# Kernel tuning notes

Hardware: AMD Instinct MI355X
Metric: run time of the kernel (lower is better)

Reference implementation:

```python
import jax, jax.numpy as jnp
import numpy as np

N_NODES = 100000
N_EDGES = 1600000
IN_CH = 64 * 2  # 128


def setup_inputs() -> dict:
    key = jax.random.key(0)
    ks = jax.random.split(key, 10)
    x = jax.random.normal(ks[0], (N_NODES, IN_CH), dtype=jnp.float32)
    edge_index = jax.random.randint(ks[1], (2, N_EDGES), 0, N_NODES, dtype=jnp.int64)
    # PyTorch Linear default init scale ~ 1/sqrt(fan_in); plain normals are fine for a numeric reference
    W1 = jax.random.normal(ks[2], (IN_CH, 64), dtype=jnp.float32) / np.sqrt(IN_CH)
    b1 = jax.random.normal(ks[3], (64,), dtype=jnp.float32) * 0.01
    W2 = jax.random.normal(ks[4], (64, 64), dtype=jnp.float32) / np.sqrt(64)
    b2 = jax.random.normal(ks[5], (64,), dtype=jnp.float32) * 0.01
    W3 = jax.random.normal(ks[6], (64, 16), dtype=jnp.float32) / np.sqrt(64)
    b3 = jax.random.normal(ks[7], (16,), dtype=jnp.float32) * 0.01
    W4 = jax.random.normal(ks[8], (16, 1), dtype=jnp.float32) / np.sqrt(16)
    b4 = jax.random.normal(ks[9], (1,), dtype=jnp.float32) * 0.01
    return {"x": x, "edge_index": edge_index, "W1": W1, "b1": b1, "W2": W2, "b2": b2,
            "W3": W3, "b3": b3, "W4": W4, "b4": b4}


def _gin_agg(h, src, dst, n):
    # GINConv (eps=0, add aggregation): x_i + sum_{j->i} x_j
    return h + jax.ops.segment_sum(h[src], dst, num_segments=n)


def reference(x, edge_index, W1, b1, W2, b2, W3, b3, W4, b4):
    src, dst = edge_index[0], edge_index[1]
    n = x.shape[0]
    h = jax.nn.relu(_gin_agg(x, src, dst, n) @ W1 + b1)   # conv1 + relu -> [N, 64]
    h = jax.nn.relu(_gin_agg(h, src, dst, n) @ W2 + b2)   # conv2 + relu -> [N, 64]
    h = jax.nn.relu(h @ W3 + b3)                          # lin1 + relu  -> [N, 16]
    return h @ W4 + b4                                    # lin2         -> [N, 1]
```

## Files before the change

### kernel.cpp

```cpp
#include <hip/hip_runtime.h>
#include <hip/hip_fp16.h>

#define N_NODES 100000
#define N_EDGES 1600000
#define NBUCK 196
#define BUCAP 10240
#define P1_EDGES 8192
#define NP1 196
#define CURPAD 32

typedef _Float16 f16x8 __attribute__((ext_vector_type(8)));
typedef float    f32x4 __attribute__((ext_vector_type(4)));

__global__ __launch_bounds__(256) void k_zero_cur(int* __restrict__ cursor) {
    if (threadIdx.x < NBUCK) cursor[threadIdx.x * CURPAD] = 0;
}

__global__ __launch_bounds__(1024) void k_p1(const int* __restrict__ ei,
                                             int* __restrict__ cursor,
                                             int* __restrict__ bArr) {
    __shared__ int hist[NBUCK];
    const int tid = threadIdx.x;
    if (tid < NBUCK) hist[tid] = 0;

    const int eb = blockIdx.x * P1_EDGES;
    int d[8], s[8];
    #pragma unroll
    for (int j = 0; j < 2; ++j) {
        const int e = eb + j * 4096 + tid * 4;
        if (e < N_EDGES) {
            int4 dd = *(const int4*)&ei[N_EDGES + e];
            int4 ss = *(const int4*)&ei[e];
            d[j*4+0] = dd.x; d[j*4+1] = dd.y; d[j*4+2] = dd.z; d[j*4+3] = dd.w;
            s[j*4+0] = ss.x; s[j*4+1] = ss.y; s[j*4+2] = ss.z; s[j*4+3] = ss.w;
        } else {
            d[j*4+0] = -1; d[j*4+1] = -1; d[j*4+2] = -1; d[j*4+3] = -1;
            s[j*4+0] = 0;  s[j*4+1] = 0;  s[j*4+2] = 0;  s[j*4+3] = 0;
        }
    }
    __syncthreads();
    #pragma unroll
    for (int j = 0; j < 8; ++j)
        if (d[j] >= 0) atomicAdd(&hist[d[j] >> 9], 1);
    __syncthreads();
    if (tid < NBUCK) {
        int c = hist[tid];
        int base = atomicAdd(&cursor[tid * CURPAD], c);
        hist[tid] = base;
    }
    __syncthreads();
    #pragma unroll
    for (int j = 0; j < 8; ++j)
        if (d[j] >= 0) {
            int bk  = d[j] >> 9;
            int pos = atomicAdd(&hist[bk], 1);
            if (pos < BUCAP)
                bArr[bk * BUCAP + pos] = ((d[j] & 511) << 17) | s[j];
        }
}

__global__ __launch_bounds__(1024) void k_p2(const int* __restrict__ bArr,
                                             const int* __restrict__ cursor,
                                             int* __restrict__ srcS,
                                             int* __restrict__ off) {
    __shared__ int hist[512];
    __shared__ int wtot[8];
    __shared__ int curL[NBUCK];
    __shared__ int ordered[BUCAP];
    const int tid = threadIdx.x;
    const int b   = blockIdx.x;
    if (tid < 512)   hist[tid] = 0;
    if (tid < NBUCK) curL[tid] = cursor[tid * CURPAD];
    __syncthreads();

    int n = curL[b]; if (n > BUCAP) n = BUCAP;
    int gBase = 0;
    for (int j = 0; j < NBUCK; ++j) gBase += (j < b) ? curL[j] : 0;

    int pk[10];
    #pragma unroll
    for (int j = 0; j < 10; ++j) {
        int i = tid + j * 1024;
        pk[j] = (i < n) ? bArr[b * BUCAP + i] : -1;
    }
    #pragma unroll
    for (int j = 0; j < 10; ++j)
        if (pk[j] >= 0) atomicAdd(&hist[pk[j] >> 17], 1);
    __syncthreads();

    int v = 0, incl = 0;
    if (tid < 512) {
        v = hist[tid]; incl = v;
        #pragma unroll
        for (int dd = 1; dd < 64; dd <<= 1) {
            int t = __shfl_up(incl, dd, 64);
            if ((tid & 63) >= dd) incl += t;
        }
        if ((tid & 63) == 63) wtot[tid >> 6] = incl;
    }
    __syncthreads();
    if (tid < 512) {
        int add = 0;
        #pragma unroll
        for (int w = 0; w < 8; ++w) add += (w < (tid >> 6)) ? wtot[w] : 0;
        int ex = add + incl - v;
        hist[tid] = ex;
        int node = b * 512 + tid;
        if (node < N_NODES) off[node] = gBase + ex;
    }
    if (b == NBUCK - 1 && tid == 0) off[N_NODES] = N_EDGES;
    __syncthreads();

    #pragma unroll
    for (int j = 0; j < 10; ++j)
        if (pk[j] >= 0) {
            int dl  = pk[j] >> 17;
            int pos = atomicAdd(&hist[dl], 1);
            ordered[pos] = pk[j] & 0x1FFFF;
        }
    __syncthreads();
    for (int i = tid; i < n; i += 1024) srcS[gBase + i] = ordered[i];
}

__device__ __forceinline__ float2 gather_core(const int* __restrict__ off,
                                              const int* __restrict__ srcS,
                                              const __half* __restrict__ y16,
                                              int node, int lane) {
    const int hf   = lane >> 5;
    const int ln32 = lane & 31;
    const int beg = off[node];
    const int end = off[node + 1];

    float2 acc = {0.f, 0.f};
    if (hf == 0) {
        __half2 hv = *(const __half2*)&y16[((size_t)node << 6) + (ln32 << 1)];
        float2 f = __half22float2(hv);
        acc.x = f.x; acc.y = f.y;
    }

    int i = beg;
    while (i < end) {
        const int rem  = end - i;
        const int take = rem < 64 ? rem : 64;
        int idx = i + lane;
        if (idx > end - 1) idx = end - 1;
        const int sv = srcS[idx];
        int j = 0;
        for (; j + 16 <= take; j += 16) {
            const int s0 = __shfl(sv, j + 0  + hf), s1 = __shfl(sv, j + 2  + hf);
            const int s2 = __shfl(sv, j + 4  + hf), s3 = __shfl(sv, j + 6  + hf);
            const int s4 = __shfl(sv, j + 8  + hf), s5 = __shfl(sv, j + 10 + hf);
            const int s6 = __shfl(sv, j + 12 + hf), s7 = __shfl(sv, j + 14 + hf);
            const __half2 h0 = *(const __half2*)&y16[((size_t)s0 << 6) + (ln32 << 1)];
            const __half2 h1 = *(const __half2*)&y16[((size_t)s1 << 6) + (ln32 << 1)];
            const __half2 h2 = *(const __half2*)&y16[((size_t)s2 << 6) + (ln32 << 1)];
            const __half2 h3 = *(const __half2*)&y16[((size_t)s3 << 6) + (ln32 << 1)];
            const __half2 h4 = *(const __half2*)&y16[((size_t)s4 << 6) + (ln32 << 1)];
            const __half2 h5 = *(const __half2*)&y16[((size_t)s5 << 6) + (ln32 << 1)];
            const __half2 h6 = *(const __half2*)&y16[((size_t)s6 << 6) + (ln32 << 1)];
            const __half2 h7 = *(const __half2*)&y16[((size_t)s7 << 6) + (ln32 << 1)];
            float2 f0 = __half22float2(h0), f1 = __half22float2(h1);
            float2 f2 = __half22float2(h2), f3 = __half22float2(h3);
            float2 f4 = __half22float2(h4), f5 = __half22float2(h5);
            float2 f6 = __half22float2(h6), f7 = __half22float2(h7);
            acc.x += ((f0.x + f1.x) + (f2.x + f3.x)) + ((f4.x + f5.x) + (f6.x + f7.x));
            acc.y += ((f0.y + f1.y) + (f2.y + f3.y)) + ((f4.y + f5.y) + (f6.y + f7.y));
        }
        for (; j + 2 <= take; j += 2) {
            const int s = __shfl(sv, j + hf);
            const __half2 hv = *(const __half2*)&y16[((size_t)s << 6) + (ln32 << 1)];
            float2 f = __half22float2(hv);
            acc.x += f.x; acc.y += f.y;
        }
        if (j < take) {
            const int s = __shfl(sv, j);
            if (hf == 0) {
                const __half2 hv = *(const __half2*)&y16[((size_t)s << 6) + (ln32 << 1)];
                float2 f = __half22float2(hv);
                acc.x += f.x; acc.y += f.y;
            }
        }
        i += take;
    }
    return acc;
}

__global__ __launch_bounds__(256) void k_gather_h1(const int* __restrict__ off,
                                                   const int* __restrict__ srcS,
                                                   const __half* __restrict__ y16,
                                                   const float* __restrict__ b1,
                                                   __half* __restrict__ h16) {
    const int node = blockIdx.x * 4 + (threadIdx.x >> 6);
    if (node >= N_NODES) return;
    const int lane = threadIdx.x & 63;
    const int hf = lane >> 5, ln32 = lane & 31;
    float2 bb = {0.f, 0.f};
    if (hf == 0) bb = *(const float2*)&b1[ln32 * 2];

    float2 acc = gather_core(off, srcS, y16, node, lane);
    acc.x += __shfl_xor(acc.x, 32, 64);
    acc.y += __shfl_xor(acc.y, 32, 64);
    if (hf == 0) {
        float hx = fmaxf(acc.x + bb.x, 0.f);
        float hy = fmaxf(acc.y + bb.y, 0.f);
        *(__half2*)&h16[((size_t)node << 6) + (ln32 << 1)] = __floats2half2_rn(hx, hy);
    }
}

__global__ __launch_bounds__(256) void k_gather_tail(const int* __restrict__ off,
                                                     const int* __restrict__ srcS,
                                                     const __half* __restrict__ y16,
                                                     const float* __restrict__ b2,
                                                     const float* __restrict__ W3,
                                                     const float* __restrict__ b3,
                                                     const float* __restrict__ W4,
                                                     const float* __restrict__ b4,
                                                     float* __restrict__ out) {
    __shared__ float sh2[4][64];
    const int wv   = threadIdx.x >> 6;
    const int node = blockIdx.x * 4 + wv;
    if (node >= N_NODES) return;
    const int lane = threadIdx.x & 63;
    const int hf = lane >> 5, ln32 = lane & 31;

    const int jj = lane & 15, pp = lane >> 4;
    float w3r[16];
    #pragma unroll
    for (int k = 0; k < 16; ++k) w3r[k] = W3[(pp * 16 + k) * 16 + jj];
    const float b3j = b3[jj], w4j = W4[jj], b4v = b4[0];
    float2 bb = {0.f, 0.f};
    if (hf == 0) bb = *(const float2*)&b2[ln32 * 2];

    float2 acc = gather_core(off, srcS, y16, node, lane);
    acc.x += __shfl_xor(acc.x, 32, 64);
    acc.y += __shfl_xor(acc.y, 32, 64);
    if (hf == 0) {
        float hx = fmaxf(acc.x + bb.x, 0.f);
        float hy = fmaxf(acc.y + bb.y, 0.f);
        *(float2*)&sh2[wv][ln32 * 2] = make_float2(hx, hy);
    }
    const float4 hA = *(const float4*)&sh2[wv][pp * 16 + 0];
    const float4 hB = *(const float4*)&sh2[wv][pp * 16 + 4];
    const float4 hC = *(const float4*)&sh2[wv][pp * 16 + 8];
    const float4 hD = *(const float4*)&sh2[wv][pp * 16 + 12];
    float part = hA.x * w3r[0]  + hA.y * w3r[1]  + hA.z * w3r[2]  + hA.w * w3r[3]
               + hB.x * w3r[4]  + hB.y * w3r[5]  + hB.z * w3r[6]  + hB.w * w3r[7]
               + hC.x * w3r[8]  + hC.y * w3r[9]  + hC.z * w3r[10] + hC.w * w3r[11]
               + hD.x * w3r[12] + hD.y * w3r[13] + hD.z * w3r[14] + hD.w * w3r[15];
    part += __shfl_xor(part, 16, 64);
    part += __shfl_xor(part, 32, 64);
    float o = fmaxf(part + b3j, 0.f) * w4j;
    o += __shfl_xor(o, 1, 64);
    o += __shfl_xor(o, 2, 64);
    o += __shfl_xor(o, 4, 64);
    o += __shfl_xor(o, 8, 64);
    if (lane == 0) out[node] = o + b4v;
}

__global__ __launch_bounds__(256) void k_mm1(const float* __restrict__ x,
                                             const float* __restrict__ W1,
                                             __half* __restrict__ y16) {
    __shared__ __half sB[64 * 136];
    const int tid = threadIdx.x;
    for (int i = tid * 4; i < 128 * 64; i += 1024) {
        int k = i >> 6, n = i & 63;
        float4 w = *(const float4*)&W1[i];
        sB[(n + 0) * 136 + k] = __float2half(w.x);
        sB[(n + 1) * 136 + k] = __float2half(w.y);
        sB[(n + 2) * 136 + k] = __float2half(w.z);
        sB[(n + 3) * 136 + k] = __float2half(w.w);
    }
    __syncthreads();
    const int wv = tid >> 6, l = tid & 63;
    const int row0 = blockIdx.x * 64 + wv * 16;
    int arow = row0 + (l & 15);
    if (arow >= N_NODES) arow = N_NODES - 1;
    const int kgrp = (l >> 4) * 8;

    f32x4 acc0 = {0,0,0,0}, acc1 = {0,0,0,0}, acc2 = {0,0,0,0}, acc3 = {0,0,0,0};
    #pragma unroll
    for (int ks = 0; ks < 4; ++ks) {
        const float4 a0 = *(const float4*)&x[(size_t)arow * 128 + ks * 32 + kgrp];
        const float4 a1 = *(const float4*)&x[(size_t)arow * 128 + ks * 32 + kgrp + 4];
        f16x8 af;
        af[0] = (_Float16)a0.x; af[1] = (_Float16)a0.y;
        af[2] = (_Float16)a0.z; af[3] = (_Float16)a0.w;
        af[4] = (_Float16)a1.x; af[5] = (_Float16)a1.y;
        af[6] = (_Float16)a1.z; af[7] = (_Float16)a1.w;
        union { uint4 u; f16x8 h; } B0, B1, B2, B3;
        B0.u = *(const uint4*)&sB[(0 * 16 + (l & 15)) * 136 + ks * 32 + kgrp];
        B1.u = *(const uint4*)&sB[(1 * 16 + (l & 15)) * 136 + ks * 32 + kgrp];
        B2.u = *(const uint4*)&sB[(2 * 16 + (l & 15)) * 136 + ks * 32 + kgrp];
        B3.u = *(const uint4*)&sB[(3 * 16 + (l & 15)) * 136 + ks * 32 + kgrp];
        acc0 = __builtin_amdgcn_mfma_f32_16x16x32_f16(af, B0.h, acc0, 0, 0, 0);
        acc1 = __builtin_amdgcn_mfma_f32_16x16x32_f16(af, B1.h, acc1, 0, 0, 0);
        acc2 = __builtin_amdgcn_mfma_f32_16x16x32_f16(af, B2.h, acc2, 0, 0, 0);
        acc3 = __builtin_amdgcn_mfma_f32_16x16x32_f16(af, B3.h, acc3, 0, 0, 0);
    }
    #pragma unroll
    for (int rr = 0; rr < 4; ++rr) {
        const int orow = row0 + (l >> 4) * 4 + rr;
        if (orow < N_NODES) {
            __half* yp = &y16[(size_t)orow * 64 + (l & 15)];
            yp[0]  = __float2half(acc0[rr]);
            yp[16] = __float2half(acc1[rr]);
            yp[32] = __float2half(acc2[rr]);
            yp[48] = __float2half(acc3[rr]);
        }
    }
}

__global__ __launch_bounds__(256) void k_mm2(const __half* __restrict__ h16,
                                             const float* __restrict__ W2,
                                             __half* __restrict__ y16) {
    __shared__ __half sB[64 * 72];
    const int tid = threadIdx.x;
    for (int i = tid * 4; i < 64 * 64; i += 1024) {
        int k = i >> 6, n = i & 63;
        float4 w = *(const float4*)&W2[i];
        sB[(n + 0) * 72 + k] = __float2half(w.x);
        sB[(n + 1) * 72 + k] = __float2half(w.y);
        sB[(n + 2) * 72 + k] = __float2half(w.z);
        sB[(n + 3) * 72 + k] = __float2half(w.w);
    }
    __syncthreads();
    const int wv = tid >> 6, l = tid & 63;
    const int row0 = blockIdx.x * 64 + wv * 16;
    int arow = row0 + (l & 15);
    if (arow >= N_NODES) arow = N_NODES - 1;
    const int kgrp = (l >> 4) * 8;

    f32x4 acc0 = {0,0,0,0}, acc1 = {0,0,0,0}, acc2 = {0,0,0,0}, acc3 = {0,0,0,0};
    #pragma unroll
    for (int ks = 0; ks < 2; ++ks) {
        union { uint4 u; f16x8 h; } A;
        A.u = *(const uint4*)&h16[(size_t)arow * 64 + ks * 32 + kgrp];
        union { uint4 u; f16x8 h; } B0, B1, B2, B3;
        B0.u = *(const uint4*)&sB[(0 * 16 + (l & 15)) * 72 + ks * 32 + kgrp];
        B1.u = *(const uint4*)&sB[(1 * 16 + (l & 15)) * 72 + ks * 32 + kgrp];
        B2.u = *(const uint4*)&sB[(2 * 16 + (l & 15)) * 72 + ks * 32 + kgrp];
        B3.u = *(const uint4*)&sB[(3 * 16 + (l & 15)) * 72 + ks * 32 + kgrp];
        acc0 = __builtin_amdgcn_mfma_f32_16x16x32_f16(A.h, B0.h, acc0, 0, 0, 0);
        acc1 = __builtin_amdgcn_mfma_f32_16x16x32_f16(A.h, B1.h, acc1, 0, 0, 0);
        acc2 = __builtin_amdgcn_mfma_f32_16x16x32_f16(A.h, B2.h, acc2, 0, 0, 0);
        acc3 = __builtin_amdgcn_mfma_f32_16x16x32_f16(A.h, B3.h, acc3, 0, 0, 0);
    }
    #pragma unroll
    for (int rr = 0; rr < 4; ++rr) {
        const int orow = row0 + (l >> 4) * 4 + rr;
        if (orow < N_NODES) {
            __half* yp = &y16[(size_t)orow * 64 + (l & 15)];
            yp[0]  = __float2half(acc0[rr]);
            yp[16] = __float2half(acc1[rr]);
            yp[32] = __float2half(acc2[rr]);
            yp[48] = __float2half(acc3[rr]);
        }
    }
}

extern "C" void kernel_launch(void* const* d_in, const int* in_sizes, int n_in,
                              void* d_out, int out_size, void* d_ws, size_t ws_size,
                              hipStream_t stream) {
    const float* x  = (const float*)d_in[0];
    const int*   ei = (const int*)d_in[1];
    const float* W1 = (const float*)d_in[2];
    const float* b1 = (const float*)d_in[3];
    const float* W2 = (const float*)d_in[4];
    const float* b2 = (const float*)d_in[5];
    const float* W3 = (const float*)d_in[6];
    const float* b3 = (const float*)d_in[7];
    const float* W4 = (const float*)d_in[8];
    const float* b4 = (const float*)d_in[9];
    float* out = (float*)d_out;

    __half* h16    = (__half*)d_ws;
    __half* y16    = h16 + (size_t)N_NODES * 64;
    int*    off    = (int*)(y16 + (size_t)N_NODES * 64);
    int*    srcS   = off + N_NODES + 4;
    int*    cursor = srcS + N_EDGES;
    int*    bArr   = (int*)d_ws;

    const int mmBlocks  = (N_NODES + 63) / 64;
    const int aggBlocks = (N_NODES + 3) / 4;

    k_zero_cur<<<1, 256, 0, stream>>>(cursor);
    k_p1<<<NP1, 1024, 0, stream>>>(ei, cursor, bArr);
    k_p2<<<NBUCK, 1024, 0, stream>>>(bArr, cursor, srcS, off);

    k_mm1<<<mmBlocks, 256, 0, stream>>>(x, W1, y16);
    k_gather_h1<<<aggBlocks, 256, 0, stream>>>(off, srcS, y16, b1, h16);
    k_mm2<<<mmBlocks, 256, 0, stream>>>(h16, W2, y16);
    k_gather_tail<<<aggBlocks, 256, 0, stream>>>(off, srcS, y16, b2, W3, b3, W4, b4, out);
}
```

Before: 254.9 us.

## Stage bucketed edges in LDS for coalesced scatter, use fp16 pair adds in gather

```diff
diff --git a/kernel.cpp b/kernel.cpp
--- a/kernel.cpp
+++ b/kernel.cpp
@@ -5,8 +5,8 @@
 #define N_EDGES 1600000
 #define NBUCK 196
 #define BUCAP 10240
-#define P1_EDGES 8192
-#define NP1 196
+#define P1_EDGES 4096
+#define NP1 391
 #define CURPAD 32
 
 typedef _Float16 f16x8 __attribute__((ext_vector_type(8)));
@@ -20,43 +20,54 @@
                                              int* __restrict__ cursor,
                                              int* __restrict__ bArr) {
     __shared__ int hist[NBUCK];
+    __shared__ int lcur[NBUCK];
+    __shared__ int gdb[NBUCK];
+    __shared__ int lim[NBUCK];
+    __shared__ int stage[P1_EDGES];
+    __shared__ int sdest[P1_EDGES];
+    __shared__ int sTot;
     const int tid = threadIdx.x;
     if (tid < NBUCK) hist[tid] = 0;
 
-    const int eb = blockIdx.x * P1_EDGES;
-    int d[8], s[8];
-    #pragma unroll
-    for (int j = 0; j < 2; ++j) {
-        const int e = eb + j * 4096 + tid * 4;
-        if (e < N_EDGES) {
-            int4 dd = *(const int4*)&ei[N_EDGES + e];
-            int4 ss = *(const int4*)&ei[e];
-            d[j*4+0] = dd.x; d[j*4+1] = dd.y; d[j*4+2] = dd.z; d[j*4+3] = dd.w;
-            s[j*4+0] = ss.x; s[j*4+1] = ss.y; s[j*4+2] = ss.z; s[j*4+3] = ss.w;
-        } else {
-            d[j*4+0] = -1; d[j*4+1] = -1; d[j*4+2] = -1; d[j*4+3] = -1;
-            s[j*4+0] = 0;  s[j*4+1] = 0;  s[j*4+2] = 0;  s[j*4+3] = 0;
-        }
-    }
-    __syncthreads();
-    #pragma unroll
-    for (int j = 0; j < 8; ++j)
+    const int e = blockIdx.x * P1_EDGES + tid * 4;
+    int4 dd = {-1, -1, -1, -1}, ss = {0, 0, 0, 0};
+    if (e < N_EDGES) {
+        dd = *(const int4*)&ei[N_EDGES + e];
+        ss = *(const int4*)&ei[e];
+    }
+    __syncthreads();
+    int d[4] = {dd.x, dd.y, dd.z, dd.w};
+    int s[4] = {ss.x, ss.y, ss.z, ss.w};
+    #pragma unroll
+    for (int j = 0; j < 4; ++j)
         if (d[j] >= 0) atomicAdd(&hist[d[j] >> 9], 1);
     __syncthreads();
     if (tid < NBUCK) {
-        int c = hist[tid];
-        int base = atomicAdd(&cursor[tid * CURPAD], c);
-        hist[tid] = base;
-    }
-    __syncthreads();
-    #pragma unroll
-    for (int j = 0; j < 8; ++j)
+        int c  = hist[tid];
+        int lb = 0;
+        for (int j = 0; j < NBUCK; ++j) lb += (j < tid) ? hist[j] : 0;
+        if (tid == NBUCK - 1) sTot = lb + c;
+        int g = atomicAdd(&cursor[tid * CURPAD], c);
+        lcur[tid] = lb;
+        gdb[tid]  = tid * BUCAP + g - lb;
+        lim[tid]  = tid * BUCAP + BUCAP;
+    }
+    __syncthreads();
+    #pragma unroll
+    for (int j = 0; j < 4; ++j)
         if (d[j] >= 0) {
-            int bk  = d[j] >> 9;
-            int pos = atomicAdd(&hist[bk], 1);
-            if (pos < BUCAP)
-                bArr[bk * BUCAP + pos] = ((d[j] & 511) << 17) | s[j];
-        }
+            int bk   = d[j] >> 9;
+            int lpos = atomicAdd(&lcur[bk], 1);
+            int dest = gdb[bk] + lpos;
+            stage[lpos] = ((d[j] & 511) << 17) | s[j];
+            sdest[lpos] = (dest < lim[bk]) ? dest : -1;
+        }
+    __syncthreads();
+    const int tot = sTot;
+    for (int i = tid; i < tot; i += 1024) {
+        int dst = sdest[i];
+        if (dst >= 0) bArr[dst] = stage[i];
+    }
 }
 
 __global__ __launch_bounds__(1024) void k_p2(const int* __restrict__ bArr,
@@ -128,12 +139,14 @@
                                               int node, int lane) {
     const int hf   = lane >> 5;
     const int ln32 = lane & 31;
+    const unsigned co = (unsigned)(ln32 << 2);
+    const char* yb = (const char*)y16;
     const int beg = off[node];
     const int end = off[node + 1];
 
     float2 acc = {0.f, 0.f};
     if (hf == 0) {
-        __half2 hv = *(const __half2*)&y16[((size_t)node << 6) + (ln32 << 1)];
+        __half2 hv = *(const __half2*)(yb + (((unsigned)node << 7) | co));
         float2 f = __half22float2(hv);
         acc.x = f.x; acc.y = f.y;
     }
@@ -151,31 +164,33 @@
             const int s2 = __shfl(sv, j + 4  + hf), s3 = __shfl(sv, j + 6  + hf);
             const int s4 = __shfl(sv, j + 8  + hf), s5 = __shfl(sv, j + 10 + hf);
             const int s6 = __shfl(sv, j + 12 + hf), s7 = __shfl(sv, j + 14 + hf);
-            const __half2 h0 = *(const __half2*)&y16[((size_t)s0 << 6) + (ln32 << 1)];
-            const __half2 h1 = *(const __half2*)&y16[((size_t)s1 << 6) + (ln32 << 1)];
-            const __half2 h2 = *(const __half2*)&y16[((size_t)s2 << 6) + (ln32 << 1)];
-            const __half2 h3 = *(const __half2*)&y16[((size_t)s3 << 6) + (ln32 << 1)];
-            const __half2 h4 = *(const __half2*)&y16[((size_t)s4 << 6) + (ln32 << 1)];
-            const __half2 h5 = *(const __half2*)&y16[((size_t)s5 << 6) + (ln32 << 1)];
-            const __half2 h6 = *(const __half2*)&y16[((size_t)s6 << 6) + (ln32 << 1)];
-            const __half2 h7 = *(const __half2*)&y16[((size_t)s7 << 6) + (ln32 << 1)];
-            float2 f0 = __half22float2(h0), f1 = __half22float2(h1);
-            float2 f2 = __half22float2(h2), f3 = __half22float2(h3);
-            float2 f4 = __half22float2(h4), f5 = __half22float2(h5);
-            float2 f6 = __half22float2(h6), f7 = __half22float2(h7);
-            acc.x += ((f0.x + f1.x) + (f2.x + f3.x)) + ((f4.x + f5.x) + (f6.x + f7.x));
-            acc.y += ((f0.y + f1.y) + (f2.y + f3.y)) + ((f4.y + f5.y) + (f6.y + f7.y));
+            const __half2 h0 = *(const __half2*)(yb + (((unsigned)s0 << 7) | co));
+            const __half2 h1 = *(const __half2*)(yb + (((unsigned)s1 << 7) | co));
+            const __half2 h2 = *(const __half2*)(yb + (((unsigned)s2 << 7) | co));
+            const __half2 h3 = *(const __half2*)(yb + (((unsigned)s3 << 7) | co));
+            const __half2 h4 = *(const __half2*)(yb + (((unsigned)s4 << 7) | co));
+            const __half2 h5 = *(const __half2*)(yb + (((unsigned)s5 << 7) | co));
+            const __half2 h6 = *(const __half2*)(yb + (((unsigned)s6 << 7) | co));
+            const __half2 h7 = *(const __half2*)(yb + (((unsigned)s7 << 7) | co));
+            const __half2 t0 = __hadd2(h0, h1);
+            const __half2 t1 = __hadd2(h2, h3);
+            const __half2 t2 = __hadd2(h4, h5);
+            const __half2 t3 = __hadd2(h6, h7);
+            float2 f0 = __half22float2(t0), f1 = __half22float2(t1);
+            float2 f2 = __half22float2(t2), f3 = __half22float2(t3);
+            acc.x += (f0.x + f1.x) + (f2.x + f3.x);
+            acc.y += (f0.y + f1.y) + (f2.y + f3.y);
         }
         for (; j + 2 <= take; j += 2) {
             const int s = __shfl(sv, j + hf);
-            const __half2 hv = *(const __half2*)&y16[((size_t)s << 6) + (ln32 << 1)];
+            const __half2 hv = *(const __half2*)(yb + (((unsigned)s << 7) | co));
             float2 f = __half22float2(hv);
             acc.x += f.x; acc.y += f.y;
         }
         if (j < take) {
             const int s = __shfl(sv, j);
             if (hf == 0) {
-                const __half2 hv = *(const __half2*)&y16[((size_t)s << 6) + (ln32 << 1)];
+                const __half2 hv = *(const __half2*)(yb + (((unsigned)s << 7) | co));
                 float2 f = __half22float2(hv);
                 acc.x += f.x; acc.y += f.y;
             }
```

New measurement: 250.8 us. Within noise of the previous version (-1.6%).

## Co-schedule CSR bucket sort with first matmul in one launch

Applied to the files above, without the earlier changes.

```diff
diff --git a/kernel.cpp b/kernel.cpp
--- a/kernel.cpp
+++ b/kernel.cpp
@@ -7,14 +7,11 @@
 #define BUCAP 10240
 #define P1_EDGES 8192
 #define NP1 196
+#define MM1_BLOCKS 391
 #define CURPAD 32
 
 typedef _Float16 f16x8 __attribute__((ext_vector_type(8)));
 typedef float    f32x4 __attribute__((ext_vector_type(4)));
-
-__global__ __launch_bounds__(256) void k_zero_cur(int* __restrict__ cursor) {
-    if (threadIdx.x < NBUCK) cursor[threadIdx.x * CURPAD] = 0;
-}
 
 __global__ __launch_bounds__(1024) void k_p1(const int* __restrict__ ei,
                                              int* __restrict__ cursor,
@@ -59,67 +56,120 @@
         }
 }
 
-__global__ __launch_bounds__(1024) void k_p2(const int* __restrict__ bArr,
-                                             const int* __restrict__ cursor,
-                                             int* __restrict__ srcS,
-                                             int* __restrict__ off) {
-    __shared__ int hist[512];
-    __shared__ int wtot[8];
-    __shared__ int curL[NBUCK];
-    __shared__ int ordered[BUCAP];
+__global__ __launch_bounds__(1024) void k_p2mm1(const int* __restrict__ bArr,
+                                                const int* __restrict__ cursor,
+                                                int* __restrict__ srcS,
+                                                int* __restrict__ off,
+                                                const float* __restrict__ x,
+                                                const float* __restrict__ W1,
+                                                __half* __restrict__ y16) {
+    __shared__ union SU {
+        struct { int hist[512]; int wtot[8]; int curL[NBUCK]; int ordered[BUCAP]; } p2;
+        __half sB[64 * 136];
+    } u;
     const int tid = threadIdx.x;
-    const int b   = blockIdx.x;
-    if (tid < 512)   hist[tid] = 0;
-    if (tid < NBUCK) curL[tid] = cursor[tid * CURPAD];
-    __syncthreads();
-
-    int n = curL[b]; if (n > BUCAP) n = BUCAP;
-    int gBase = 0;
-    for (int j = 0; j < NBUCK; ++j) gBase += (j < b) ? curL[j] : 0;
-
-    int pk[10];
-    #pragma unroll
-    for (int j = 0; j < 10; ++j) {
-        int i = tid + j * 1024;
-        pk[j] = (i < n) ? bArr[b * BUCAP + i] : -1;
-    }
-    #pragma unroll
-    for (int j = 0; j < 10; ++j)
-        if (pk[j] >= 0) atomicAdd(&hist[pk[j] >> 17], 1);
-    __syncthreads();
-
-    int v = 0, incl = 0;
-    if (tid < 512) {
-        v = hist[tid]; incl = v;
-        #pragma unroll
-        for (int dd = 1; dd < 64; dd <<= 1) {
-            int t = __shfl_up(incl, dd, 64);
-            if ((tid & 63) >= dd) incl += t;
-        }
-        if ((tid & 63) == 63) wtot[tid >> 6] = incl;
-    }
-    __syncthreads();
-    if (tid < 512) {
-        int add = 0;
-        #pragma unroll
-        for (int w = 0; w < 8; ++w) add += (w < (tid >> 6)) ? wtot[w] : 0;
-        int ex = add + incl - v;
-        hist[tid] = ex;
-        int node = b * 512 + tid;
-        if (node < N_NODES) off[node] = gBase + ex;
-    }
-    if (b == NBUCK - 1 && tid == 0) off[N_NODES] = N_EDGES;
-    __syncthreads();
-
-    #pragma unroll
-    for (int j = 0; j < 10; ++j)
-        if (pk[j] >= 0) {
-            int dl  = pk[j] >> 17;
-            int pos = atomicAdd(&hist[dl], 1);
-            ordered[pos] = pk[j] & 0x1FFFF;
-        }
-    __syncthreads();
-    for (int i = tid; i < n; i += 1024) srcS[gBase + i] = ordered[i];
+
+    if (blockIdx.x < NBUCK) {
+        const int b = blockIdx.x;
+        if (tid < 512)   u.p2.hist[tid] = 0;
+        if (tid < NBUCK) u.p2.curL[tid] = cursor[tid * CURPAD];
+        __syncthreads();
+
+        int n = u.p2.curL[b]; if (n > BUCAP) n = BUCAP;
+        int gBase = 0;
+        for (int j = 0; j < NBUCK; ++j) gBase += (j < b) ? u.p2.curL[j] : 0;
+
+        int pk[10];
+        #pragma unroll
+        for (int j = 0; j < 10; ++j) {
+            int i = tid + j * 1024;
+            pk[j] = (i < n) ? bArr[b * BUCAP + i] : -1;
+        }
+        #pragma unroll
+        for (int j = 0; j < 10; ++j)
+            if (pk[j] >= 0) atomicAdd(&u.p2.hist[pk[j] >> 17], 1);
+        __syncthreads();
+
+        int v = 0, incl = 0;
+        if (tid < 512) {
+            v = u.p2.hist[tid]; incl = v;
+            #pragma unroll
+            for (int dd = 1; dd < 64; dd <<= 1) {
+                int t = __shfl_up(incl, dd, 64);
+                if ((tid & 63) >= dd) incl += t;
+            }
+            if ((tid & 63) == 63) u.p2.wtot[tid >> 6] = incl;
+        }
+        __syncthreads();
+        if (tid < 512) {
+            int add = 0;
+            #pragma unroll
+            for (int w = 0; w < 8; ++w) add += (w < (tid >> 6)) ? u.p2.wtot[w] : 0;
+            int ex = add + incl - v;
+            u.p2.hist[tid] = ex;
+            int node = b * 512 + tid;
+            if (node < N_NODES) off[node] = gBase + ex;
+        }
+        if (b == NBUCK - 1 && tid == 0) off[N_NODES] = N_EDGES;
+        __syncthreads();
+
+        #pragma unroll
+        for (int j = 0; j < 10; ++j)
+            if (pk[j] >= 0) {
+                int dl  = pk[j] >> 17;
+                int pos = atomicAdd(&u.p2.hist[dl], 1);
+                u.p2.ordered[pos] = pk[j] & 0x1FFFF;
+            }
+        __syncthreads();
+        for (int i = tid; i < n; i += 1024) srcS[gBase + i] = u.p2.ordered[i];
+    } else {
+        for (int i = tid * 4; i < 128 * 64; i += 4096) {
+            int k = i >> 6, nn = i & 63;
+            float4 w = *(const float4*)&W1[i];
+            u.sB[(nn + 0) * 136 + k] = __float2half(w.x);
+            u.sB[(nn + 1) * 136 + k] = __float2half(w.y);
+            u.sB[(nn + 2) * 136 + k] = __float2half(w.z);
+            u.sB[(nn + 3) * 136 + k] = __float2half(w.w);
+        }
+        __syncthreads();
+        const int wv = tid >> 6, l = tid & 63;
+        const int row0 = (blockIdx.x - NBUCK) * 256 + wv * 16;
+        int arow = row0 + (l & 15);
+        if (arow >= N_NODES) arow = N_NODES - 1;
+        const int kgrp = (l >> 4) * 8;
+
+        f32x4 acc0 = {0,0,0,0}, acc1 = {0,0,0,0}, acc2 = {0,0,0,0}, acc3 = {0,0,0,0};
+        #pragma unroll
+        for (int ks = 0; ks < 4; ++ks) {
+            const float4 a0 = *(const float4*)&x[(size_t)arow * 128 + ks * 32 + kgrp];
+            const float4 a1 = *(const float4*)&x[(size_t)arow * 128 + ks * 32 + kgrp + 4];
+            f16x8 af;
+            af[0] = (_Float16)a0.x; af[1] = (_Float16)a0.y;
+            af[2] = (_Float16)a0.z; af[3] = (_Float16)a0.w;
+            af[4] = (_Float16)a1.x; af[5] = (_Float16)a1.y;
+            af[6] = (_Float16)a1.z; af[7] = (_Float16)a1.w;
+            union { uint4 q; f16x8 h; } B0, B1, B2, B3;
+            B0.q = *(const uint4*)&u.sB[(0 * 16 + (l & 15)) * 136 + ks * 32 + kgrp];
+            B1.q = *(const uint4*)&u.sB[(1 * 16 + (l & 15)) * 136 + ks * 32 + kgrp];
+            B2.q = *(const uint4*)&u.sB[(2 * 16 + (l & 15)) * 136 + ks * 32 + kgrp];
+            B3.q = *(const uint4*)&u.sB[(3 * 16 + (l & 15)) * 136 + ks * 32 + kgrp];
+            acc0 = __builtin_amdgcn_mfma_f32_16x16x32_f16(af, B0.h, acc0, 0, 0, 0);
+            acc1 = __builtin_amdgcn_mfma_f32_16x16x32_f16(af, B1.h, acc1, 0, 0, 0);
+            acc2 = __builtin_amdgcn_mfma_f32_16x16x32_f16(af, B2.h, acc2, 0, 0, 0);
+            acc3 = __builtin_amdgcn_mfma_f32_16x16x32_f16(af, B3.h, acc3, 0, 0, 0);
+        }
+        #pragma unroll
+        for (int rr = 0; rr < 4; ++rr) {
+            const int orow = row0 + (l >> 4) * 4 + rr;
+            if (orow < N_NODES) {
+                __half* yp = &y16[(size_t)orow * 64 + (l & 15)];
+                yp[0]  = __float2half(acc0[rr]);
+                yp[16] = __float2half(acc1[rr]);
+                yp[32] = __float2half(acc2[rr]);
+                yp[48] = __float2half(acc3[rr]);
+            }
+        }
+    }
 }
 
 __device__ __forceinline__ float2 gather_core(const int* __restrict__ off,
@@ -128,12 +178,14 @@
                                               int node, int lane) {
     const int hf   = lane >> 5;
     const int ln32 = lane & 31;
+    const unsigned co = (unsigned)(ln32 << 2);
+    const char* yb = (const char*)y16;
     const int beg = off[node];
     const int end = off[node + 1];
 
     float2 acc = {0.f, 0.f};
     if (hf == 0) {
-        __half2 hv = *(const __half2*)&y16[((size_t)node << 6) + (ln32 << 1)];
+        __half2 hv = *(const __half2*)(yb + (((unsigned)node << 7) | co));
         float2 f = __half22float2(hv);
         acc.x = f.x; acc.y = f.y;
     }
@@ -151,31 +203,33 @@
             const int s2 = __shfl(sv, j + 4  + hf), s3 = __shfl(sv, j + 6  + hf);
             const int s4 = __shfl(sv, j + 8  + hf), s5 = __shfl(sv, j + 10 + hf);
             const int s6 = __shfl(sv, j + 12 + hf), s7 = __shfl(sv, j + 14 + hf);
-            const __half2 h0 = *(const __half2*)&y16[((size_t)s0 << 6) + (ln32 << 1)];
-            const __half2 h1 = *(const __half2*)&y16[((size_t)s1 << 6) + (ln32 << 1)];
-            const __half2 h2 = *(const __half2*)&y16[((size_t)s2 << 6) + (ln32 << 1)];
-            const __half2 h3 = *(const __half2*)&y16[((size_t)s3 << 6) + (ln32 << 1)];
-            const __half2 h4 = *(const __half2*)&y16[((size_t)s4 << 6) + (ln32 << 1)];
-            const __half2 h5 = *(const __half2*)&y16[((size_t)s5 << 6) + (ln32 << 1)];
-            const __half2 h6 = *(const __half2*)&y16[((size_t)s6 << 6) + (ln32 << 1)];
-            const __half2 h7 = *(const __half2*)&y16[((size_t)s7 << 6) + (ln32 << 1)];
-            float2 f0 = __half22float2(h0), f1 = __half22float2(h1);
-            float2 f2 = __half22float2(h2), f3 = __half22float2(h3);
-            float2 f4 = __half22float2(h4), f5 = __half22float2(h5);
-            float2 f6 = __half22float2(h6), f7 = __half22float2(h7);
-            acc.x += ((f0.x + f1.x) + (f2.x + f3.x)) + ((f4.x + f5.x) + (f6.x + f7.x));
-            acc.y += ((f0.y + f1.y) + (f2.y + f3.y)) + ((f4.y + f5.y) + (f6.y + f7.y));
+            const __half2 h0 = *(const __half2*)(yb + (((unsigned)s0 << 7) | co));
+            const __half2 h1 = *(const __half2*)(yb + (((unsigned)s1 << 7) | co));
+            const __half2 h2 = *(const __half2*)(yb + (((unsigned)s2 << 7) | co));
+            const __half2 h3 = *(const __half2*)(yb + (((unsigned)s3 << 7) | co));
+            const __half2 h4 = *(const __half2*)(yb + (((unsigned)s4 << 7) | co));
+            const __half2 h5 = *(const __half2*)(yb + (((unsigned)s5 << 7) | co));
+            const __half2 h6 = *(const __half2*)(yb + (((unsigned)s6 << 7) | co));
+            const __half2 h7 = *(const __half2*)(yb + (((unsigned)s7 << 7) | co));
+            const __half2 t0 = __hadd2(h0, h1);
+            const __half2 t1 = __hadd2(h2, h3);
+            const __half2 t2 = __hadd2(h4, h5);
+            const __half2 t3 = __hadd2(h6, h7);
+            float2 f0 = __half22float2(t0), f1 = __half22float2(t1);
+            float2 f2 = __half22float2(t2), f3 = __half22float2(t3);
+            acc.x += (f0.x + f1.x) + (f2.x + f3.x);
+            acc.y += (f0.y + f1.y) + (f2.y + f3.y);
         }
         for (; j + 2 <= take; j += 2) {
             const int s = __shfl(sv, j + hf);
-            const __half2 hv = *(const __half2*)&y16[((size_t)s << 6) + (ln32 << 1)];
+            const __half2 hv = *(const __half2*)(yb + (((unsigned)s << 7) | co));
             float2 f = __half22float2(hv);
             acc.x += f.x; acc.y += f.y;
         }
         if (j < take) {
             const int s = __shfl(sv, j);
             if (hf == 0) {
-                const __half2 hv = *(const __half2*)&y16[((size_t)s << 6) + (ln32 << 1)];
+                const __half2 hv = *(const __half2*)(yb + (((unsigned)s << 7) | co));
                 float2 f = __half22float2(hv);
                 acc.x += f.x; acc.y += f.y;
             }
@@ -257,59 +311,6 @@
     if (lane == 0) out[node] = o + b4v;
 }
 
-__global__ __launch_bounds__(256) void k_mm1(const float* __restrict__ x,
-                                             const float* __restrict__ W1,
-                                             __half* __restrict__ y16) {
-    __shared__ __half sB[64 * 136];
-    const int tid = threadIdx.x;
-    for (int i = tid * 4; i < 128 * 64; i += 1024) {
-        int k = i >> 6, n = i & 63;
-        float4 w = *(const float4*)&W1[i];
-        sB[(n + 0) * 136 + k] = __float2half(w.x);
-        sB[(n + 1) * 136 + k] = __float2half(w.y);
-        sB[(n + 2) * 136 + k] = __float2half(w.z);
-        sB[(n + 3) * 136 + k] = __float2half(w.w);
-    }
-    __syncthreads();
-    const int wv = tid >> 6, l = tid & 63;
-    const int row0 = blockIdx.x * 64 + wv * 16;
-    int arow = row0 + (l & 15);
-    if (arow >= N_NODES) arow = N_NODES - 1;
-    const int kgrp = (l >> 4) * 8;
-
-    f32x4 acc0 = {0,0,0,0}, acc1 = {0,0,0,0}, acc2 = {0,0,0,0}, acc3 = {0,0,0,0};
-    #pragma unroll
-    for (int ks = 0; ks < 4; ++ks) {
-        const float4 a0 = *(const float4*)&x[(size_t)arow * 128 + ks * 32 + kgrp];
-        const float4 a1 = *(const float4*)&x[(size_t)arow * 128 + ks * 32 + kgrp + 4];
-        f16x8 af;
-        af[0] = (_Float16)a0.x; af[1] = (_Float16)a0.y;
-        af[2] = (_Float16)a0.z; af[3] = (_Float16)a0.w;
-        af[4] = (_Float16)a1.x; af[5] = (_Float16)a1.y;
-        af[6] = (_Float16)a1.z; af[7] = (_Float16)a1.w;
-        union { uint4 u; f16x8 h; } B0, B1, B2, B3;
-        B0.u = *(const uint4*)&sB[(0 * 16 + (l & 15)) * 136 + ks * 32 + kgrp];
-        B1.u = *(const uint4*)&sB[(1 * 16 + (l & 15)) * 136 + ks * 32 + kgrp];
-        B2.u = *(const uint4*)&sB[(2 * 16 + (l & 15)) * 136 + ks * 32 + kgrp];
-        B3.u = *(const uint4*)&sB[(3 * 16 + (l & 15)) * 136 + ks * 32 + kgrp];
-        acc0 = __builtin_amdgcn_mfma_f32_16x16x32_f16(af, B0.h, acc0, 0, 0, 0);
-        acc1 = __builtin_amdgcn_mfma_f32_16x16x32_f16(af, B1.h, acc1, 0, 0, 0);
-        acc2 = __builtin_amdgcn_mfma_f32_16x16x32_f16(af, B2.h, acc2, 0, 0, 0);
-        acc3 = __builtin_amdgcn_mfma_f32_16x16x32_f16(af, B3.h, acc3, 0, 0, 0);
-    }
-    #pragma unroll
-    for (int rr = 0; rr < 4; ++rr) {
-        const int orow = row0 + (l >> 4) * 4 + rr;
-        if (orow < N_NODES) {
-            __half* yp = &y16[(size_t)orow * 64 + (l & 15)];
-            yp[0]  = __float2half(acc0[rr]);
-            yp[16] = __float2half(acc1[rr]);
-            yp[32] = __float2half(acc2[rr]);
-            yp[48] = __float2half(acc3[rr]);
-        }
-    }
-}
-
 __global__ __launch_bounds__(256) void k_mm2(const __half* __restrict__ h16,
                                              const float* __restrict__ W2,
                                              __half* __restrict__ y16) {
@@ -333,13 +334,13 @@
     f32x4 acc0 = {0,0,0,0}, acc1 = {0,0,0,0}, acc2 = {0,0,0,0}, acc3 = {0,0,0,0};
     #pragma unroll
     for (int ks = 0; ks < 2; ++ks) {
-        union { uint4 u; f16x8 h; } A;
-        A.u = *(const uint4*)&h16[(size_t)arow * 64 + ks * 32 + kgrp];
-        union { uint4 u; f16x8 h; } B0, B1, B2, B3;
-        B0.u = *(const uint4*)&sB[(0 * 16 + (l & 15)) * 72 + ks * 32 + kgrp];
-        B1.u = *(const uint4*)&sB[(1 * 16 + (l & 15)) * 72 + ks * 32 + kgrp];
-        B2.u = *(const uint4*)&sB[(2 * 16 + (l & 15)) * 72 + ks * 32 + kgrp];
-        B3.u = *(const uint4*)&sB[(3 * 16 + (l & 15)) * 72 + ks * 32 + kgrp];
+        union { uint4 q; f16x8 h; } A;
+        A.q = *(const uint4*)&h16[(size_t)arow * 64 + ks * 32 + kgrp];
+        union { uint4 q; f16x8 h; } B0, B1, B2, B3;
+        B0.q = *(const uint4*)&sB[(0 * 16 + (l & 15)) * 72 + ks * 32 + kgrp];
+        B1.q = *(const uint4*)&sB[(1 * 16 + (l & 15)) * 72 + ks * 32 + kgrp];
+        B2.q = *(const uint4*)&sB[(2 * 16 + (l & 15)) * 72 + ks * 32 + kgrp];
+        B3.q = *(const uint4*)&sB[(3 * 16 + (l & 15)) * 72 + ks * 32 + kgrp];
         acc0 = __builtin_amdgcn_mfma_f32_16x16x32_f16(A.h, B0.h, acc0, 0, 0, 0);
         acc1 = __builtin_amdgcn_mfma_f32_16x16x32_f16(A.h, B1.h, acc1, 0, 0, 0);
         acc2 = __builtin_amdgcn_mfma_f32_16x16x32_f16(A.h, B2.h, acc2, 0, 0, 0);
@@ -383,11 +384,11 @@
     const int mmBlocks  = (N_NODES + 63) / 64;
     const int aggBlocks = (N_NODES + 3) / 4;
 
-    k_zero_cur<<<1, 256, 0, stream>>>(cursor);
+    hipMemsetAsync(cursor, 0, NBUCK * CURPAD * sizeof(int), stream);
     k_p1<<<NP1, 1024, 0, stream>>>(ei, cursor, bArr);
-    k_p2<<<NBUCK, 1024, 0, stream>>>(bArr, cursor, srcS, off);
-
-    k_mm1<<<mmBlocks, 256, 0, stream>>>(x, W1, y16);
+    k_p2mm1<<<NBUCK + MM1_BLOCKS, 1024, 0, stream>>>(bArr, cursor, srcS, off,
+                                                     x, W1, y16);
+
     k_gather_h1<<<aggBlocks, 256, 0, stream>>>(off, srcS, y16, b1, h16);
     k_mm2<<<mmBlocks, 256, 0, stream>>>(h16, W2, y16);
     k_gather_tail<<<aggBlocks, 256, 0, stream>>>(off, srcS, y16, b2, W3, b3, W4, b4, out);
```

Measured after the change: 241.8 us. 5.1% less time.
